# Optimization experiments

Hardware: AMD Instinct MI355X
Metric: run time of the kernel (lower is better)

Reference implementation:

```python
import jax, jax.numpy as jnp
import numpy as np

RADIUS = 0.1
NSAMPLE = 32


def ball_query(xyz, new_xyz, radius, nsample):
    """xyz:(B,N,3), new_xyz:(B,P,3) -> idx:(B,P,nsample) int32.
    Semantics of PointNet++ CUDA ball_query: first `nsample` points (in index
    order) within `radius`; remaining slots padded with the first found index
    (0 if no point is within radius)."""
    d2 = jnp.sum((new_xyz[:, :, None, :] - xyz[:, None, :, :]) ** 2, axis=-1)  # (B,P,N)
    mask = d2 < radius * radius
    cnt = jnp.cumsum(mask, axis=-1) - 1               # rank of each hit
    valid = mask & (cnt < nsample)
    first = jnp.argmax(mask, axis=-1)                 # first in-ball index (0 if none)
    B, P, N = d2.shape
    pos = jnp.where(valid, cnt, nsample)              # invalid -> dump slot
    buf = jnp.broadcast_to(first[..., None], (B, P, nsample + 1))
    j = jnp.broadcast_to(jnp.arange(N)[None, None, :], (B, P, N))
    b = jnp.arange(B)[:, None, None]
    p = jnp.arange(P)[None, :, None]
    buf = buf.at[b, p, pos].set(j)
    return buf[..., :nsample].astype(jnp.int32)


def setup_inputs() -> dict:
    key = jax.random.key(0)
    k1, k2, k3 = jax.random.split(key, 3)
    xyz = jax.random.uniform(k1, (2, 16384, 3), dtype=jnp.float32)
    new_xyz = jax.random.uniform(k2, (2, 4096, 3), dtype=jnp.float32)
    features = jax.random.normal(k3, (2, 64, 16384), dtype=jnp.float32)
    return {"xyz": xyz, "new_xyz": new_xyz, "features": features}


def reference(xyz, new_xyz, features):
    idx = ball_query(xyz, new_xyz, RADIUS, NSAMPLE)              # (B,P,S)
    grouped_xyz = jax.vmap(lambda x, i: x[i])(xyz, idx)          # (B,P,S,3)
    grouped_xyz = jnp.transpose(grouped_xyz, (0, 3, 1, 2))       # (B,3,P,S)
    grouped_xyz = grouped_xyz - jnp.transpose(new_xyz, (0, 2, 1))[..., None]
    grouped_feat = jax.vmap(lambda f, i: f[:, i])(features, idx) # (B,C,P,S)
    return jnp.concatenate([grouped_xyz, grouped_feat], axis=1)  # (B,3+C,P,S)
```

## Files before the change

### kernel.cpp

```cpp
#include <hip/hip_runtime.h>
#include <hip/hip_bf16.h>
#include <climits>

#define BATCH   2
#define NPTS    16384
#define NQ      4096
#define CFEAT   64
#define NS      32
#define R2      0.01f
#define COUT    (3 + CFEAT)
#define GDIM    10
#define NCELL   (GDIM * GDIM * GDIM)
#define NWORDS  (NPTS / 32)

#define FEATT_BYTES ((size_t)BATCH * NPTS * CFEAT * sizeof(unsigned short))
#define PXYZJ_BYTES ((size_t)BATCH * NPTS * sizeof(float4))
#define OFF_CNT    0
#define OFF_FILL   (2 * NCELL)
#define OFF_CSTART (4 * NCELL)
#define GRID_INTS  (4 * NCELL + 2 * (NCELL + 1))

__device__ __forceinline__ int cell_of(float x, float y, float z) {
    int cx = (int)(x * GDIM); cx = cx < 0 ? 0 : (cx > GDIM - 1 ? GDIM - 1 : cx);
    int cy = (int)(y * GDIM); cy = cy < 0 ? 0 : (cy > GDIM - 1 ? GDIM - 1 : cy);
    int cz = (int)(z * GDIM); cz = cz < 0 ? 0 : (cz > GDIM - 1 ? GDIM - 1 : cz);
    return (cz * GDIM + cy) * GDIM + cx;
}

__device__ __forceinline__ unsigned short f2bf(float f) {
    unsigned b = __float_as_uint(f);
    return (unsigned short)((b + 0x7FFFu + ((b >> 16) & 1u)) >> 16);
}
__device__ __forceinline__ float bflo(unsigned u) { return __uint_as_float(u << 16); }
__device__ __forceinline__ float bfhi(unsigned u) { return __uint_as_float(u & 0xFFFF0000u); }

__global__ __launch_bounds__(256) void prep1_kernel(
    const float* __restrict__ feat, unsigned short* __restrict__ featT16,
    const float* __restrict__ xyz, int* __restrict__ cnt)
{
    __shared__ float tile[64][65];
    if (blockIdx.x < 512) {
        const int b    = blockIdx.x >> 8;
        const int n0   = (blockIdx.x & 255) * 64;
        const int lane = threadIdx.x & 63;
        const int grp  = threadIdx.x >> 6;
        const float* fb = feat + (size_t)b * CFEAT * NPTS;
        #pragma unroll
        for (int k = 0; k < 16; ++k) {
            const int c = grp * 16 + k;
            tile[c][lane] = fb[(size_t)c * NPTS + n0 + lane];
        }
        __syncthreads();
        unsigned short* db = featT16 + ((size_t)b * NPTS + n0) * CFEAT;
        #pragma unroll
        for (int k = 0; k < 8; ++k) {
            const int e   = threadIdx.x + 256 * k;
            const int row = e >> 5;
            const int c2  = e & 31;
            ushort2 v;
            v.x = f2bf(tile[2 * c2][row]);
            v.y = f2bf(tile[2 * c2 + 1][row]);
            ((ushort2*)(db + (size_t)row * CFEAT))[c2] = v;
        }
    } else {
        const int g = (blockIdx.x - 512) * 256 + threadIdx.x;
        const int b = g >> 14;
        const int c = cell_of(xyz[g*3], xyz[g*3+1], xyz[g*3+2]);
        atomicAdd(&cnt[b * NCELL + c], 1);
    }
}

__global__ __launch_bounds__(256) void prep2_kernel(
    const float* __restrict__ xyz, const int* __restrict__ cnt,
    int* __restrict__ fill, int* __restrict__ cstart,
    float4* __restrict__ pxyzj)
{
    __shared__ int scs[2 * NCELL];
    const int tid  = threadIdx.x;
    const int lane = tid & 63;

    if (tid < 128) {
        const int b = tid >> 6;
        int c16[16];
        int tot = 0;
        #pragma unroll
        for (int k = 0; k < 16; ++k) {
            const int i = lane * 16 + k;
            c16[k] = (i < NCELL) ? cnt[b * NCELL + i] : 0;
            tot += c16[k];
        }
        int ex = tot;
        #pragma unroll
        for (int off = 1; off < 64; off <<= 1) {
            const int u = __shfl_up(ex, off);
            if (lane >= off) ex += u;
        }
        ex -= tot;
        int run = ex;
        #pragma unroll
        for (int k = 0; k < 16; ++k) {
            const int i = lane * 16 + k;
            if (i < NCELL) scs[b * NCELL + i] = run;
            run += c16[k];
        }
    }
    __syncthreads();

    if (blockIdx.x == 0) {
        for (int i = tid; i < 2 * (NCELL + 1); i += 256) {
            const int b  = i / (NCELL + 1);
            const int ci = i - b * (NCELL + 1);
            cstart[i] = (ci == NCELL) ? NPTS : scs[b * NCELL + ci];
        }
    }

    const int g = blockIdx.x * 256 + tid;
    const int b = g >> 14;
    const int j = g & (NPTS - 1);
    const float x = xyz[g*3], y = xyz[g*3+1], z = xyz[g*3+2];
    const int c = cell_of(x, y, z);
    const int pos = atomicAdd(&fill[b * NCELL + c], 1);
    pxyzj[b * NPTS + scs[b * NCELL + c] + pos] =
        make_float4(x, y, z, __int_as_float(j));
}

__global__ __launch_bounds__(128) void qg_fused(
    const float* __restrict__ xyz,
    const float* __restrict__ new_xyz,
    const int* __restrict__ cstart,
    const float4* __restrict__ pxyzj,
    const unsigned short* __restrict__ featT16,
    float* __restrict__ out)
{
    const int q    = blockIdx.x;
    const int b    = q >> 12;
    const int p    = q & (NQ - 1);
    const int tid  = threadIdx.x;
    const int wave = tid >> 6;
    const int lane = tid & 63;

    __shared__ __align__(16) unsigned char smem[NS * 65 * sizeof(float)];
    unsigned int* hmask = (unsigned int*)smem;
    float (*tile)[65]   = (float(*)[65])smem;
    __shared__ int idx_s[NS];

    {
        uint4 z; z.x = 0; z.y = 0; z.z = 0; z.w = 0;
        ((uint4*)hmask)[tid] = z;
    }

    const float qx = new_xyz[q * 3 + 0];
    const float qy = new_xyz[q * 3 + 1];
    const float qz = new_xyz[q * 3 + 2];
    const float* xb = xyz + (size_t)b * NPTS * 3;
    const int* cs = cstart + b * (NCELL + 1);
    const float4* pb = pxyzj + (size_t)b * NPTS;

    int qcx = (int)(qx * GDIM); qcx = qcx < 0 ? 0 : (qcx > GDIM-1 ? GDIM-1 : qcx);
    int qcy = (int)(qy * GDIM); qcy = qcy < 0 ? 0 : (qcy > GDIM-1 ? GDIM-1 : qcy);
    int qcz = (int)(qz * GDIM); qcz = qcz < 0 ? 0 : (qcz > GDIM-1 ? GDIM-1 : qcz);
    const int x0 = qcx > 0 ? qcx - 1 : 0;
    const int x1 = qcx < GDIM-1 ? qcx + 1 : GDIM-1;
    const int y0 = qcy > 0 ? qcy - 1 : 0;
    const int y1 = qcy < GDIM-1 ? qcy + 1 : GDIM-1;
    const int z0 = qcz > 0 ? qcz - 1 : 0;
    const int z1 = qcz < GDIM-1 ? qcz + 1 : GDIM-1;
    const int ny  = y1 - y0 + 1;
    const int nyz = ny * (z1 - z0 + 1);

    int sv = 0, ev = 0;
    if (lane < nyz) {
        const int gzi = (ny == 3) ? ((lane * 86) >> 8) : (lane >> 1);
        const int gyi = lane - gzi * ny;
        const int crow = ((z0 + gzi) * GDIM + (y0 + gyi)) * GDIM;
        sv = cs[crow + x0];
        ev = cs[crow + x1 + 1];
    }
    __syncthreads();

    for (int r = wave; r < nyz; r += 2) {
        const int s = __shfl(sv, r);
        const int e = __shfl(ev, r);
        for (int pos = s; pos < e; pos += 64) {
            const int i = pos + lane;
            const bool inr = i < e;
            const float4 pt = pb[inr ? i : 0];
            const float dx = pt.x - qx;
            const float dy = pt.y - qy;
            const float dz = pt.z - qz;
            if (inr && (dx*dx + dy*dy + dz*dz < R2)) {
                const int j = __float_as_int(pt.w);
                atomicOr(&hmask[j >> 5], 1u << (j & 31));
            }
        }
    }
    __syncthreads();

    {
        unsigned int w[8];
        const uint4 a = ((const uint4*)hmask)[lane * 2];
        const uint4 c = ((const uint4*)hmask)[lane * 2 + 1];
        w[0] = a.x; w[1] = a.y; w[2] = a.z; w[3] = a.w;
        w[4] = c.x; w[5] = c.y; w[6] = c.z; w[7] = c.w;

        int cnt8 = 0;
        #pragma unroll
        for (int k = 0; k < 8; ++k) cnt8 += __popc(w[k]);

        int pfx = cnt8;
        #pragma unroll
        for (int off = 1; off < 64; off <<= 1) {
            const int u = __shfl_up(pfx, off);
            if (lane >= off) pfx += u;
        }
        const int K = __shfl(pfx, 63);
        pfx -= cnt8;

        if (pfx < NS && cnt8 > 0) {
            int r = pfx;
            #pragma unroll
            for (int k = 0; k < 8; ++k) {
                unsigned int m = w[k];
                while (m && r < NS) {
                    const int bit = __builtin_ctz(m);
                    idx_s[r] = lane * 256 + k * 32 + bit;
                    m &= m - 1;
                    ++r;
                }
            }
        }
        __builtin_amdgcn_wave_barrier();
        if (lane < NS && lane >= K) {
            idx_s[lane] = (K > 0) ? idx_s[0] : 0;
        }
        __builtin_amdgcn_wave_barrier();
    }

    const int sm = tid >> 2;
    const int q4 = tid & 3;
    const unsigned short* base16 = featT16 + ((size_t)b * NPTS + idx_s[sm]) * CFEAT;
    const uint4 va = ((const uint4*)base16)[q4 * 2];
    const uint4 vb = ((const uint4*)base16)[q4 * 2 + 1];

    const size_t cstride = (size_t)NQ * NS;
    const size_t out_q   = ((size_t)b * COUT * NQ + (size_t)p) * NS;

    float xv = 0.f, yv = 0.f, zv = 0.f;
    if (tid < NS) {
        const int j = idx_s[tid];
        xv = xb[j*3+0] - qx;
        yv = xb[j*3+1] - qy;
        zv = xb[j*3+2] - qz;
    }
    __syncthreads();

    float4 f0, f1, f2, f3;
    f0.x = bflo(va.x); f0.y = bfhi(va.x); f0.z = bflo(va.y); f0.w = bfhi(va.y);
    f1.x = bflo(va.z); f1.y = bfhi(va.z); f1.z = bflo(va.w); f1.w = bfhi(va.w);
    f2.x = bflo(vb.x); f2.y = bfhi(vb.x); f2.z = bflo(vb.y); f2.w = bfhi(vb.y);
    f3.x = bflo(vb.z); f3.y = bfhi(vb.z); f3.z = bflo(vb.w); f3.w = bfhi(vb.w);
    ((float4*)&tile[sm][q4 * 16])[0]      = f0;
    ((float4*)&tile[sm][q4 * 16 + 4])[0]  = f1;
    ((float4*)&tile[sm][q4 * 16 + 8])[0]  = f2;
    ((float4*)&tile[sm][q4 * 16 + 12])[0] = f3;

    if (tid < NS) {
        out[out_q + 0*cstride + tid] = xv;
        out[out_q + 1*cstride + tid] = yv;
        out[out_q + 2*cstride + tid] = zv;
    }
    __syncthreads();

    const int s  = tid & 31;
    const int c4 = tid >> 5;
    float* ob = out + out_q + s + 3 * cstride;
    #pragma unroll
    for (int k = 0; k < 16; ++k) {
        const int c = c4 + k * 4;
        ob[(size_t)c * cstride] = tile[s][c];
    }
}

__global__ __launch_bounds__(256) void qg_linear(
    const float* __restrict__ xyz, const float* __restrict__ new_xyz,
    const float* __restrict__ feat, float* __restrict__ out)
{
    const int wave = threadIdx.x >> 6;
    const int lane = threadIdx.x & 63;
    const int bp   = blockIdx.x * 4 + wave;
    const int b    = bp >> 12;
    const int p    = bp & (NQ - 1);
    __shared__ int idx_s[4][NS];
    const float qx = new_xyz[bp*3+0], qy = new_xyz[bp*3+1], qz = new_xyz[bp*3+2];
    const float* xb = xyz + (size_t)b * NPTS * 3;
    int cnt = 0;
    const unsigned long long below = (1ull << lane) - 1ull;
    for (int base = 0; base < NPTS; base += 64) {
        const int j = base + lane;
        const float dx = xb[j*3+0]-qx, dy = xb[j*3+1]-qy, dz = xb[j*3+2]-qz;
        const bool hit = dx*dx+dy*dy+dz*dz < R2;
        const unsigned long long m = __ballot(hit);
        if (hit) {
            const int slot = cnt + __popcll(m & below);
            if (slot < NS) idx_s[wave][slot] = j;
        }
        cnt += __popcll(m);
        if (cnt >= NS) break;
    }
    __builtin_amdgcn_wave_barrier();
    if (cnt < NS) {
        const int first = (cnt > 0) ? idx_s[wave][0] : 0;
        if (lane >= cnt && lane < NS) idx_s[wave][lane] = first;
    }
    __builtin_amdgcn_wave_barrier();
    const size_t cstride = (size_t)NQ * NS;
    const size_t out_q = ((size_t)b * COUT * NQ + (size_t)p) * NS;
    if (lane < NS) {
        const int j = idx_s[wave][lane];
        out[out_q + 0*cstride + lane] = xb[j*3+0] - qx;
        out[out_q + 1*cstride + lane] = xb[j*3+1] - qy;
        out[out_q + 2*cstride + lane] = xb[j*3+2] - qz;
    }
    const float* fb = feat + (size_t)b * CFEAT * NPTS;
    const int s = lane & 31, half = lane >> 5;
    const int j = idx_s[wave][s];
    #pragma unroll 8
    for (int c = half; c < CFEAT; c += 2)
        out[out_q + (size_t)(3 + c) * cstride + s] = fb[(size_t)c * NPTS + j];
}

extern "C" void kernel_launch(void* const* d_in, const int* in_sizes, int n_in,
                              void* d_out, int out_size, void* d_ws, size_t ws_size,
                              hipStream_t stream) {
    const float* xyz     = (const float*)d_in[0];
    const float* new_xyz = (const float*)d_in[1];
    const float* feat    = (const float*)d_in[2];
    float* out = (float*)d_out;

    const size_t need_full = FEATT_BYTES + PXYZJ_BYTES + (size_t)GRID_INTS * sizeof(int);

    if (ws_size >= need_full) {
        unsigned short* featT16 = (unsigned short*)d_ws;
        float4* pxyzj = (float4*)((char*)d_ws + FEATT_BYTES);
        int* gi = (int*)((char*)d_ws + FEATT_BYTES + PXYZJ_BYTES);
        int* cnt    = gi + OFF_CNT;
        int* fill   = gi + OFF_FILL;
        int* cstart = gi + OFF_CSTART;

        hipMemsetAsync(cnt, 0, 4 * NCELL * sizeof(int), stream);
        prep1_kernel<<<512 + (BATCH * NPTS) / 256, 256, 0, stream>>>(feat, featT16, xyz, cnt);
        prep2_kernel<<<(BATCH * NPTS) / 256, 256, 0, stream>>>(xyz, cnt, fill, cstart, pxyzj);
        qg_fused<<<BATCH * NQ, 128, 0, stream>>>(
            xyz, new_xyz, cstart, pxyzj, featT16, out);
    } else {
        qg_linear<<<(BATCH * NQ) / 4, 256, 0, stream>>>(xyz, new_xyz, feat, out);
    }
}
```

Baseline: 112.8 us.

## Map one query per wave and write features directly without LDS transpose

The fused query-and-group kernel now handles four queries per 256-thread block, one per wave, so block-wide barriers become wave barriers and each wave scans all neighbour cell rows by itself. The shared-memory transpose tile is gone: each lane loads half a bf16 feature row and writes 32 channels straight to global memory, with 32 lanes covering the 32 samples of one channel. This cuts block-level synchronisation and LDS traffic. In exchange, each wave does twice the scanning work of the old two-wave split, and each store instruction covers only 128 contiguous bytes per channel.

```diff
diff --git a/kernel.cpp b/kernel.cpp
--- a/kernel.cpp
+++ b/kernel.cpp
@@ -31,8 +31,6 @@
     unsigned b = __float_as_uint(f);
     return (unsigned short)((b + 0x7FFFu + ((b >> 16) & 1u)) >> 16);
 }
-__device__ __forceinline__ float bflo(unsigned u) { return __uint_as_float(u << 16); }
-__device__ __forceinline__ float bfhi(unsigned u) { return __uint_as_float(u & 0xFFFF0000u); }
 
 __global__ __launch_bounds__(256) void prep1_kernel(
     const float* __restrict__ feat, unsigned short* __restrict__ featT16,
@@ -124,7 +122,7 @@
         make_float4(x, y, z, __int_as_float(j));
 }
 
-__global__ __launch_bounds__(128) void qg_fused(
+__global__ __launch_bounds__(256) void qg_fused(
     const float* __restrict__ xyz,
     const float* __restrict__ new_xyz,
     const int* __restrict__ cstart,
@@ -132,21 +130,22 @@
     const unsigned short* __restrict__ featT16,
     float* __restrict__ out)
 {
-    const int q    = blockIdx.x;
-    const int b    = q >> 12;
-    const int p    = q & (NQ - 1);
     const int tid  = threadIdx.x;
     const int wave = tid >> 6;
     const int lane = tid & 63;
-
-    __shared__ __align__(16) unsigned char smem[NS * 65 * sizeof(float)];
-    unsigned int* hmask = (unsigned int*)smem;
-    float (*tile)[65]   = (float(*)[65])smem;
-    __shared__ int idx_s[NS];
+    const int q    = (blockIdx.x << 2) + wave;
+    const int b    = q >> 12;
+    const int p    = q & (NQ - 1);
+
+    __shared__ __align__(16) unsigned char smem[4 * 2176];
+    unsigned char* wbase = smem + wave * 2176;
+    unsigned int* hmask  = (unsigned int*)wbase;
+    int* idx_s           = (int*)(wbase + 2048);
 
     {
         uint4 z; z.x = 0; z.y = 0; z.z = 0; z.w = 0;
-        ((uint4*)hmask)[tid] = z;
+        ((uint4*)hmask)[lane * 2]     = z;
+        ((uint4*)hmask)[lane * 2 + 1] = z;
     }
 
     const float qx = new_xyz[q * 3 + 0];
@@ -176,9 +175,9 @@
         sv = cs[crow + x0];
         ev = cs[crow + x1 + 1];
     }
-    __syncthreads();
-
-    for (int r = wave; r < nyz; r += 2) {
+    __builtin_amdgcn_wave_barrier();
+
+    for (int r = 0; r < nyz; ++r) {
         const int s = __shfl(sv, r);
         const int e = __shfl(ev, r);
         for (int pos = s; pos < e; pos += 64) {
@@ -194,8 +193,9 @@
             }
         }
     }
-    __syncthreads();
-
+    __builtin_amdgcn_wave_barrier();
+
+    int K;
     {
         unsigned int w[8];
         const uint4 a = ((const uint4*)hmask)[lane * 2];
@@ -213,7 +213,7 @@
             const int u = __shfl_up(pfx, off);
             if (lane >= off) pfx += u;
         }
-        const int K = __shfl(pfx, 63);
+        K = __shfl(pfx, 63);
         pfx -= cnt8;
 
         if (pfx < NS && cnt8 > 0) {
@@ -236,48 +236,36 @@
         __builtin_amdgcn_wave_barrier();
     }
 
-    const int sm = tid >> 2;
-    const int q4 = tid & 3;
-    const unsigned short* base16 = featT16 + ((size_t)b * NPTS + idx_s[sm]) * CFEAT;
-    const uint4 va = ((const uint4*)base16)[q4 * 2];
-    const uint4 vb = ((const uint4*)base16)[q4 * 2 + 1];
+    const int sm = lane >> 1;
+    const int h  = lane & 1;
+    const int jrow = idx_s[sm];
+    const uint4* bptr = (const uint4*)(featT16 +
+        ((size_t)b * NPTS + jrow) * CFEAT + (h << 5));
+    const uint4 ga = bptr[0];
+    const uint4 gb = bptr[1];
+    const uint4 gc = bptr[2];
+    const uint4 gd = bptr[3];
 
     const size_t cstride = (size_t)NQ * NS;
     const size_t out_q   = ((size_t)b * COUT * NQ + (size_t)p) * NS;
 
-    float xv = 0.f, yv = 0.f, zv = 0.f;
-    if (tid < NS) {
-        const int j = idx_s[tid];
-        xv = xb[j*3+0] - qx;
-        yv = xb[j*3+1] - qy;
-        zv = xb[j*3+2] - qz;
-    }
-    __syncthreads();
-
-    float4 f0, f1, f2, f3;
-    f0.x = bflo(va.x); f0.y = bfhi(va.x); f0.z = bflo(va.y); f0.w = bfhi(va.y);
-    f1.x = bflo(va.z); f1.y = bfhi(va.z); f1.z = bflo(va.w); f1.w = bfhi(va.w);
-    f2.x = bflo(vb.x); f2.y = bfhi(vb.x); f2.z = bflo(vb.y); f2.w = bfhi(vb.y);
-    f3.x = bflo(vb.z); f3.y = bfhi(vb.z); f3.z = bflo(vb.w); f3.w = bfhi(vb.w);
-    ((float4*)&tile[sm][q4 * 16])[0]      = f0;
-    ((float4*)&tile[sm][q4 * 16 + 4])[0]  = f1;
-    ((float4*)&tile[sm][q4 * 16 + 8])[0]  = f2;
-    ((float4*)&tile[sm][q4 * 16 + 12])[0] = f3;
-
-    if (tid < NS) {
-        out[out_q + 0*cstride + tid] = xv;
-        out[out_q + 1*cstride + tid] = yv;
-        out[out_q + 2*cstride + tid] = zv;
-    }
-    __syncthreads();
-
-    const int s  = tid & 31;
-    const int c4 = tid >> 5;
-    float* ob = out + out_q + s + 3 * cstride;
+    if (lane < NS) {
+        const int j = idx_s[lane];
+        out[out_q + 0*cstride + lane] = xb[j*3+0] - qx;
+        out[out_q + 1*cstride + lane] = xb[j*3+1] - qy;
+        out[out_q + 2*cstride + lane] = xb[j*3+2] - qz;
+    }
+
+    float* fob = out + out_q + (size_t)(3 + (h << 5)) * cstride + sm;
+    const unsigned comps[16] = {ga.x, ga.y, ga.z, ga.w,
+                                gb.x, gb.y, gb.z, gb.w,
+                                gc.x, gc.y, gc.z, gc.w,
+                                gd.x, gd.y, gd.z, gd.w};
     #pragma unroll
-    for (int k = 0; k < 16; ++k) {
-        const int c = c4 + k * 4;
-        ob[(size_t)c * cstride] = tile[s][c];
+    for (int kk = 0; kk < 16; ++kk) {
+        const unsigned u = comps[kk];
+        fob[(size_t)(2*kk)     * cstride] = __uint_as_float(u << 16);
+        fob[(size_t)(2*kk + 1) * cstride] = __uint_as_float(u & 0xFFFF0000u);
     }
 }
 
@@ -350,7 +338,7 @@
         hipMemsetAsync(cnt, 0, 4 * NCELL * sizeof(int), stream);
         prep1_kernel<<<512 + (BATCH * NPTS) / 256, 256, 0, stream>>>(feat, featT16, xyz, cnt);
         prep2_kernel<<<(BATCH * NPTS) / 256, 256, 0, stream>>>(xyz, cnt, fill, cstart, pxyzj);
-        qg_fused<<<BATCH * NQ, 128, 0, stream>>>(
+        qg_fused<<<(BATCH * NQ) / 4, 256, 0, stream>>>(
             xyz, new_xyz, cstart, pxyzj, featT16, out);
     } else {
         qg_linear<<<(BATCH * NQ) / 4, 256, 0, stream>>>(xyz, new_xyz, feat, out);
```

After: 113.1 us. No clear change (+0.3%).
